# Performance work log

Hardware: AMD Instinct MI355X
Metric: run time of the kernel (lower is better)

Reference implementation:

```python
import jax, jax.numpy as jnp
import numpy as np

N_LAYERS = 6
D_MODEL = 512
D_FFN = 2048
N_STATE = 64
KSIZE = 31
BATCH = 8
SEQ = 2048
IN_SIZE = 80


def _ln(x, g, b, eps=1e-5):
    m = jnp.mean(x, axis=-1, keepdims=True)
    v = jnp.mean((x - m) ** 2, axis=-1, keepdims=True)
    return (x - m) * jax.lax.rsqrt(v + eps) * g + b


def _ffn(x, g, b, w1, b1, w2, b2):
    # LayerNorm -> Linear(D->F) -> GELU -> Linear(F->D)  (PositionalwiseFeedForward)
    h = jax.nn.gelu(_ln(x, g, b) @ w1 + b1)
    return h @ w2 + b2


def _dss(x, lam_re, lam_im, c_re, c_im, d_skip, log_dt, w_out, b_out):
    # Diagonal state-space (DSS-EXP): generate length-T kernel from diagonal poles,
    # apply causal conv via FFT, skip D*u, GELU, GLU output projection.
    Bx, T, H = x.shape
    dt = jnp.exp(log_dt)
    lam = -jnp.exp(lam_re) + 1j * lam_im                        # [N] stable poles (Re<0)
    P = jnp.exp(lam[:, None] * (dt * jnp.arange(T))[None, :])   # [N, T]
    C = c_re + 1j * c_im                                        # [H, N]
    kern = jnp.einsum('hn,nt->ht', C, P).real * dt              # [H, T]
    u = x.transpose(0, 2, 1)                                    # [B, H, T]
    n = 2 * T
    y = jnp.fft.irfft(jnp.fft.rfft(u, n=n) * jnp.fft.rfft(kern, n=n), n=n)[..., :T]
    y = y + d_skip[None, :, None] * u
    y = jax.nn.gelu(y.transpose(0, 2, 1))                       # [B, T, H]
    z = y @ w_out + b_out                                       # [B, T, 2H]
    a, g = jnp.split(z, 2, axis=-1)
    return a * jax.nn.sigmoid(g)                                # GLU


def _conv_module(x, g1, b1, bw, bb, dw, db, g2, b2, lw, lb):
    # LN -> 1x1 conv to 2D + GLU -> depthwise conv (SAME, k=31) -> LN -> GELU -> Linear
    y = _ln(x, g1, b1)
    y = y @ bw.T + bb                                           # [B, T, 2D]
    a, g = jnp.split(y, 2, axis=-1)
    y = a * jax.nn.sigmoid(g)                                   # GLU over channels
    yc = y.transpose(0, 2, 1)                                   # [B, D, T]
    yc = jax.lax.conv_general_dilated(
        yc, dw[:, None, :], (1,), 'SAME',
        feature_group_count=yc.shape[1],
        dimension_numbers=('NCH', 'OIH', 'NCH'))
    yc = yc + db[None, :, None]
    y = jax.nn.gelu(_ln(yc.transpose(0, 2, 1), g2, b2))
    return y @ lw.T + lb


def _forward(src, speaker_embs, src_w, src_b,
             ffn1_ln_g, ffn1_ln_b, ffn1_w1, ffn1_b1, ffn1_w2, ffn1_b2,
             norm1_g, norm1_b,
             lam_re, lam_im, c_re, c_im, ssm_d, log_dt, dss_out_w, dss_out_b,
             conv_ln_g, conv_ln_b, bneck_w, bneck_b, dw_w, dw_b,
             conv_ln2_g, conv_ln2_b, conv_lin_w, conv_lin_b,
             ffn2_ln_g, ffn2_ln_b, ffn2_w1, ffn2_b1, ffn2_w2, ffn2_b2,
             norm2_g, norm2_b, final_g, final_b):
    x = src @ src_w + src_b                                     # custom_src_module Linear
    for i in range(N_LAYERS):
        x = x + 0.5 * _ffn(x, ffn1_ln_g[i], ffn1_ln_b[i], ffn1_w1[i], ffn1_b1[i], ffn1_w2[i], ffn1_b2[i])
        skip = x
        x = _ln(x, norm1_g[i], norm1_b[i])
        x = _dss(x, lam_re[i], lam_im[i], c_re[i], c_im[i], ssm_d[i], log_dt[i], dss_out_w[i], dss_out_b[i])
        x = x + skip
        x = x + _conv_module(x, conv_ln_g[i], conv_ln_b[i], bneck_w[i], bneck_b[i], dw_w[i], dw_b[i],
                             conv_ln2_g[i], conv_ln2_b[i], conv_lin_w[i], conv_lin_b[i])
        x = _ln(x + 0.5 * _ffn(x, ffn2_ln_g[i], ffn2_ln_b[i], ffn2_w1[i], ffn2_b1[i], ffn2_w2[i], ffn2_b2[i]),
                norm2_g[i], norm2_b[i])
    x = _ln(x, final_g, final_b, eps=1e-6)
    return x + speaker_embs


def setup_inputs() -> dict:
    key = jax.random.key(0)
    ks = iter(jax.random.split(key, 64))
    def rn(shape, s=0.02):
        return (jax.random.normal(next(ks), shape) * s).astype(jnp.float32)
    L, D, F, N, K = N_LAYERS, D_MODEL, D_FFN, N_STATE, KSIZE
    return dict(
        src=jax.random.normal(next(ks), (BATCH, SEQ, IN_SIZE), dtype=jnp.float32),
        speaker_embs=jax.random.normal(next(ks), (BATCH, 1, D), dtype=jnp.float32),
        src_w=rn((IN_SIZE, D)), src_b=jnp.zeros((D,), jnp.float32),
        ffn1_ln_g=jnp.ones((L, D), jnp.float32), ffn1_ln_b=jnp.zeros((L, D), jnp.float32),
        ffn1_w1=rn((L, D, F)), ffn1_b1=jnp.zeros((L, F), jnp.float32),
        ffn1_w2=rn((L, F, D)), ffn1_b2=jnp.zeros((L, D), jnp.float32),
        norm1_g=jnp.ones((L, D), jnp.float32), norm1_b=jnp.zeros((L, D), jnp.float32),
        lam_re=rn((L, N), 0.5), lam_im=rn((L, N), 3.0),
        c_re=rn((L, D, N), 0.1), c_im=rn((L, D, N), 0.1),
        ssm_d=rn((L, D), 1.0), log_dt=jnp.full((L,), float(np.log(0.01)), jnp.float32),
        dss_out_w=rn((L, D, 2 * D)), dss_out_b=jnp.zeros((L, 2 * D), jnp.float32),
        conv_ln_g=jnp.ones((L, D), jnp.float32), conv_ln_b=jnp.zeros((L, D), jnp.float32),
        bneck_w=rn((L, 2 * D, D)), bneck_b=jnp.zeros((L, 2 * D), jnp.float32),
        dw_w=rn((L, D, K), 0.1), dw_b=jnp.zeros((L, D), jnp.float32),
        conv_ln2_g=jnp.ones((L, D), jnp.float32), conv_ln2_b=jnp.zeros((L, D), jnp.float32),
        conv_lin_w=rn((L, D, D)), conv_lin_b=jnp.zeros((L, D), jnp.float32),
        ffn2_ln_g=jnp.ones((L, D), jnp.float32), ffn2_ln_b=jnp.zeros((L, D), jnp.float32),
        ffn2_w1=rn((L, D, F)), ffn2_b1=jnp.zeros((L, F), jnp.float32),
        ffn2_w2=rn((L, F, D)), ffn2_b2=jnp.zeros((L, D), jnp.float32),
        norm2_g=jnp.ones((L, D), jnp.float32), norm2_b=jnp.zeros((L, D), jnp.float32),
        final_g=jnp.ones((D,), jnp.float32), final_b=jnp.zeros((D,), jnp.float32),
    )


def reference(src, speaker_embs, src_w, src_b,
              ffn1_ln_g, ffn1_ln_b, ffn1_w1, ffn1_b1, ffn1_w2, ffn1_b2,
              norm1_g, norm1_b,
              lam_re, lam_im, c_re, c_im, ssm_d, log_dt, dss_out_w, dss_out_b,
              conv_ln_g, conv_ln_b, bneck_w, bneck_b, dw_w, dw_b,
              conv_ln2_g, conv_ln2_b, conv_lin_w, conv_lin_b,
              ffn2_ln_g, ffn2_ln_b, ffn2_w1, ffn2_b1, ffn2_w2, ffn2_b2,
              norm2_g, norm2_b, final_g, final_b):
    return _forward(src, speaker_embs, src_w, src_b,
                    ffn1_ln_g, ffn1_ln_b, ffn1_w1, ffn1_b1, ffn1_w2, ffn1_b2,
                    norm1_g, norm1_b,
                    lam_re, lam_im, c_re, c_im, ssm_d, log_dt, dss_out_w, dss_out_b,
                    conv_ln_g, conv_ln_b, bneck_w, bneck_b, dw_w, dw_b,
                    conv_ln2_g, conv_ln2_b, conv_lin_w, conv_lin_b,
                    ffn2_ln_g, ffn2_ln_b, ffn2_w1, ffn2_b1, ffn2_w2, ffn2_b2,
                    norm2_g, norm2_b, final_g, final_b)
```

## Files before the change

kernel.cpp:

```cpp
#include <hip/hip_runtime.h>
#include <hip/hip_bf16.h>
#include <stdint.h>


#define NL 6
#define TT 2048
#define BB 8
#define DD 512
#define FF 2048
#define ROWS (BB*TT)

typedef __attribute__((ext_vector_type(4))) float f32x4;
typedef __attribute__((ext_vector_type(8))) short s16x8;

#define DEVI __device__ __forceinline__

DEVI float bf2f(uint32_t u) { union { uint32_t i; float f; } v; v.i = u << 16; return v.f; }
DEVI uint16_t f2bf(float f) {
    union { float f; uint32_t i; } v; v.f = f;
    uint32_t x = v.i;
    return (uint16_t)((x + 0x7fffu + ((x >> 16) & 1u)) >> 16);
}
DEVI float gelu_f(float x) {
    float x2 = x * x;
    float z  = x * fmaf(x2, 0.07135481627f, 1.5957691216f);
    return x * __builtin_amdgcn_rcpf(1.0f + __expf(-z));
}
DEVI float sigm(float x) { return __builtin_amdgcn_rcpf(1.0f + __expf(-x)); }

DEVI void gload16(const uint16_t* g, uint16_t* l) {
    __builtin_amdgcn_global_load_lds((const __attribute__((address_space(1))) void*)g,
                                     (__attribute__((address_space(3))) void*)l, 16, 0, 0);
}

__global__ void k_wtrans(const float* __restrict__ src, uint16_t* __restrict__ dst,
                         int K, int N) {
    __shared__ float tile[32][33];
    int l = blockIdx.z;
    const float* s = src + (size_t)l * K * N;
    uint16_t*    d = dst + (size_t)l * N * K;
    int n0 = blockIdx.x * 32, k0 = blockIdx.y * 32;
    int tx = threadIdx.x, ty = threadIdx.y;
#pragma unroll
    for (int i = 0; i < 4; i++) {
        int k = k0 + ty + i * 8;
        tile[ty + i * 8][tx] = s[(size_t)k * N + n0 + tx];
    }
    __syncthreads();
#pragma unroll
    for (int i = 0; i < 4; i++) {
        int n = n0 + ty + i * 8;
        d[(size_t)n * K + k0 + tx] = f2bf(tile[tx][ty + i * 8]);
    }
}
__global__ void k_wcvt(const float* __restrict__ src, uint16_t* __restrict__ dst, int n) {
    int i = blockIdx.x * 256 + threadIdx.x;
    if (i < n) dst[i] = f2bf(src[i]);
}
__global__ void k_dwt(const float* __restrict__ dw, float* __restrict__ dwt) {
    int i = blockIdx.x * 256 + threadIdx.x;
    int tot = NL * DD * 31;
    if (i >= tot) return;
    int l = i / (DD * 31), r = i % (DD * 31), d = r / 31, k = r % 31;
    dwt[(size_t)l * 31 * DD + k * DD + d] = dw[i];
}
__global__ void k_srcpad(const float* __restrict__ src, uint16_t* __restrict__ dst) {
    int i = blockIdx.x * 256 + threadIdx.x;
    if (i >= ROWS * 96) return;
    int r = i / 96, c = i - r * 96;
    dst[i] = (c < 80) ? f2bf(src[(size_t)r * 80 + c]) : (uint16_t)0;
}
__global__ void k_wsrcpad(const float* __restrict__ w, uint16_t* __restrict__ dst) {
    int i = blockIdx.x * 256 + threadIdx.x;
    if (i >= DD * 96) return;
    int n = i / 96, k = i - n * 96;
    dst[i] = (k < 80) ? f2bf(w[(size_t)k * DD + n]) : (uint16_t)0;
}

template <int MODE>
__global__ void k_ln(const float* __restrict__ in, void* __restrict__ outp,
                     const float* __restrict__ gam, const float* __restrict__ bet,
                     const float* __restrict__ spk, float eps) {
    int row  = blockIdx.x * 4 + (threadIdx.x >> 6);
    int lane = threadIdx.x & 63;
    const float* x = in + (size_t)row * DD;
    float4 a0 = *(const float4*)&x[lane * 4];
    float4 a1 = *(const float4*)&x[256 + lane * 4];
    float v[8] = {a0.x, a0.y, a0.z, a0.w, a1.x, a1.y, a1.z, a1.w};
    float s = 0.f, q = 0.f;
#pragma unroll
    for (int i = 0; i < 8; i++) { s += v[i]; q += v[i] * v[i]; }
#pragma unroll
    for (int m = 1; m < 64; m <<= 1) { s += __shfl_xor(s, m); q += __shfl_xor(q, m); }
    float mean = s * (1.0f / 512.0f);
    float var  = fmaxf(q * (1.0f / 512.0f) - mean * mean, 0.0f);
    float inv  = rsqrtf(var + eps);
    float4 g0 = *(const float4*)&gam[lane * 4];
    float4 g1 = *(const float4*)&gam[256 + lane * 4];
    float4 b0 = *(const float4*)&bet[lane * 4];
    float4 b1 = *(const float4*)&bet[256 + lane * 4];
    float gv[8] = {g0.x, g0.y, g0.z, g0.w, g1.x, g1.y, g1.z, g1.w};
    float bv[8] = {b0.x, b0.y, b0.z, b0.w, b1.x, b1.y, b1.z, b1.w};
    float y[8];
#pragma unroll
    for (int i = 0; i < 8; i++) y[i] = (v[i] - mean) * inv * gv[i] + bv[i];
    if (MODE == 1) {
#pragma unroll
        for (int i = 0; i < 8; i++) y[i] = gelu_f(y[i]);
    }
    if (MODE == 0 || MODE == 1) {
        uint16_t* o = (uint16_t*)outp + (size_t)row * DD;
        uint2 p0, p1;
        p0.x = (uint32_t)f2bf(y[0]) | ((uint32_t)f2bf(y[1]) << 16);
        p0.y = (uint32_t)f2bf(y[2]) | ((uint32_t)f2bf(y[3]) << 16);
        p1.x = (uint32_t)f2bf(y[4]) | ((uint32_t)f2bf(y[5]) << 16);
        p1.y = (uint32_t)f2bf(y[6]) | ((uint32_t)f2bf(y[7]) << 16);
        *(uint2*)&o[lane * 4]       = p0;
        *(uint2*)&o[256 + lane * 4] = p1;
    } else {
        float* o = (float*)outp + (size_t)row * DD;
        if (MODE == 3) {
            const float* sp = spk + (size_t)(row >> 11) * DD;
            float4 s0 = *(const float4*)&sp[lane * 4];
            float4 s1 = *(const float4*)&sp[256 + lane * 4];
            y[0] += s0.x; y[1] += s0.y; y[2] += s0.z; y[3] += s0.w;
            y[4] += s1.x; y[5] += s1.y; y[6] += s1.z; y[7] += s1.w;
        }
        *(float4*)&o[lane * 4]       = make_float4(y[0], y[1], y[2], y[3]);
        *(float4*)&o[256 + lane * 4] = make_float4(y[4], y[5], y[6], y[7]);
    }
}

template <int MODE>
__global__ __launch_bounds__(256) void k_gemm(
    const uint16_t* __restrict__ A, const uint16_t* __restrict__ Bt,
    const float* __restrict__ bias, int M, int N, int K,
    void* __restrict__ outp, float* __restrict__ X) {
    __shared__ __align__(16) uint16_t As[2][128 * 32];
    __shared__ __align__(16) uint16_t Bs[2][128 * 32];
    int tid = threadIdx.x;
    int m0 = blockIdx.x * 128, n0 = blockIdx.y * 128;
    int wave = tid >> 6, lane = tid & 63;
    int wm = (wave >> 1) * 64, wn = (wave & 1) * 64;
    int l15 = lane & 15, l16 = lane >> 4;

    const uint16_t* gA = A  + (size_t)(m0 + 32 * wave + l15) * K + l16 * 8;
    const uint16_t* gB = Bt + (size_t)(n0 + 32 * wave + l15) * K + l16 * 8;
    size_t rowskip = (size_t)16 * K;

    f32x4 acc[4][4];
#pragma unroll
    for (int i = 0; i < 4; i++)
#pragma unroll
        for (int j = 0; j < 4; j++) acc[i][j] = (f32x4){0.f, 0.f, 0.f, 0.f};

    gload16(gA, &As[0][(2 * wave) * 512]);
    gload16(gA + rowskip, &As[0][(2 * wave + 1) * 512]);
    gload16(gB, &Bs[0][(2 * wave) * 512]);
    gload16(gB + rowskip, &Bs[0][(2 * wave + 1) * 512]);
    __syncthreads();

    int nk = K >> 5;
    for (int it = 0; it < nk; ++it) {
        int cur = it & 1;
        if (it + 1 < nk) {
            int kt = (it + 1) << 5;
            gload16(gA + kt, &As[cur ^ 1][(2 * wave) * 512]);
            gload16(gA + rowskip + kt, &As[cur ^ 1][(2 * wave + 1) * 512]);
            gload16(gB + kt, &Bs[cur ^ 1][(2 * wave) * 512]);
            gload16(gB + rowskip + kt, &Bs[cur ^ 1][(2 * wave + 1) * 512]);
        }
        s16x8 af[4], bfr[4];
#pragma unroll
        for (int i = 0; i < 4; i++)
            af[i] = *(const s16x8*)&As[cur][((wave >> 1) * 4 + i) * 512 + lane * 8];
#pragma unroll
        for (int j = 0; j < 4; j++)
            bfr[j] = *(const s16x8*)&Bs[cur][((wave & 1) * 4 + j) * 512 + lane * 8];
#pragma unroll
        for (int i = 0; i < 4; i++)
#pragma unroll
            for (int j = 0; j < 4; j++)
                acc[i][j] = __builtin_amdgcn_mfma_f32_16x16x32_bf16(af[i], bfr[j], acc[i][j], 0, 0, 0);
        __syncthreads();
    }
#pragma unroll
    for (int i = 0; i < 4; i++) {
#pragma unroll
        for (int j = 0; j < 4; j++) {
            int gcol = n0 + wn + j * 16 + l15;
            float bv = bias[gcol];
#pragma unroll
            for (int q = 0; q < 4; q++) {
                int grow = m0 + wm + i * 16 + l16 * 4 + q;
                float v = acc[i][j][q] + bv;
                if (MODE == 0) {
                    ((uint16_t*)outp)[(size_t)grow * N + gcol] = f2bf(gelu_f(v));
                } else if (MODE == 1) {
                    ((uint16_t*)outp)[(size_t)grow * N + gcol] = f2bf(v);
                } else if (MODE == 2) {
                    X[(size_t)grow * DD + gcol] += 0.5f * v;
                } else if (MODE == 3) {
                    X[(size_t)grow * DD + gcol] += v;
                } else if (MODE == 4) {
                    ((float*)outp)[(size_t)grow * DD + gcol] =
                        X[(size_t)grow * DD + gcol] + 0.5f * v;
                } else {
                    X[(size_t)grow * DD + gcol] = v;
                }
            }
        }
    }
}

__global__ void k_tpose(const uint16_t* __restrict__ in, uint16_t* __restrict__ out,
                        int R, int C) {
    __shared__ uint16_t tile[32][33];
    size_t boff = (size_t)blockIdx.z * R * C;
    int c0 = blockIdx.x * 32, r0 = blockIdx.y * 32;
    int tx = threadIdx.x, ty = threadIdx.y;
#pragma unroll
    for (int i = 0; i < 4; i++)
        tile[ty + i * 8][tx] = in[boff + (size_t)(r0 + ty + i * 8) * C + c0 + tx];
    __syncthreads();
#pragma unroll
    for (int i = 0; i < 4; i++)
        out[boff + (size_t)(c0 + ty + i * 8) * R + r0 + tx] = tile[tx][ty + i * 8];
}


__global__ __launch_bounds__(64) void k_phiprep(
        const float* __restrict__ lam_re, const float* __restrict__ lam_im,
        const float* __restrict__ log_dt, uint16_t* __restrict__ PHI,
        float* __restrict__ A64f) {
    int l = blockIdx.x, n = threadIdx.x;
    float dt = expf(log_dt[l]);
    float lr = lam_re[l * 64 + n], li = lam_im[l * 64 + n];
    float mag = expf(-expf(lr) * dt), th = li * dt;
    float Are = mag * __cosf(th), Aim = mag * __sinf(th);
    float Pre = 1.f, Pim = 0.f;
    uint16_t* ph = PHI + (size_t)l * 8192;
    for (int tau = 0; tau < 64; tau++) {
        int s = 63 - tau;
        ph[n * 64 + s]        = f2bf(Pre);
        ph[(64 + n) * 64 + s] = f2bf(Pim);
        float nr = Pre * Are - Pim * Aim;
        float ni = Pre * Aim + Pim * Are;
        Pre = nr; Pim = ni;
    }
    A64f[l * 128 + 2 * n]     = Pre;
    A64f[l * 128 + 2 * n + 1] = Pim;
}

__global__ __launch_bounds__(64) void k_gprep(
        const float* __restrict__ lam_re, const float* __restrict__ lam_im,
        const float* __restrict__ c_re, const float* __restrict__ c_im,
        const float* __restrict__ ssm_d, const float* __restrict__ log_dt,
        int l, uint16_t* __restrict__ G) {
    int h = blockIdx.x, n = threadIdx.x;
    __shared__ float klds[64];
    float dt = expf(log_dt[l]);
    float lr = lam_re[l * 64 + n], li = lam_im[l * 64 + n];
    float mag = expf(-expf(lr) * dt), th = li * dt;
    float Are = mag * __cosf(th), Aim = mag * __sinf(th);
    float Cre = c_re[(size_t)l * DD * 64 + h * 64 + n];
    float Cim = c_im[(size_t)l * DD * 64 + h * 64 + n];
    uint16_t* Gh = G + (size_t)h * 64 * 192;
    float Pre = 1.f, Pim = 0.f;
    for (int r = 0; r < 64; r++) {
        float t = Cre * Pre - Cim * Pim;
        float s = t;
        s += __shfl_xor(s, 1);  s += __shfl_xor(s, 2);  s += __shfl_xor(s, 4);
        s += __shfl_xor(s, 8);  s += __shfl_xor(s, 16); s += __shfl_xor(s, 32);
        if (n == 0) klds[r] = dt * s;
        float nr = Pre * Are - Pim * Aim;
        float ni = Pre * Aim + Pim * Are;
        float wre = dt * (Cre * nr - Cim * ni);
        float wim = dt * (Cre * ni + Cim * nr);
        Gh[r * 192 + 64 + n]  = f2bf(wre);
        Gh[r * 192 + 128 + n] = f2bf(-wim);
        Pre = nr; Pim = ni;
    }
    __syncthreads();
    float dh = ssm_d[l * DD + h];
    for (int r = 0; r < 64; r++) {
        int c = n;
        float val = (c < r) ? klds[r - c] : (c == r ? klds[0] + dh : 0.f);
        Gh[r * 192 + c] = f2bf(val);
    }
}

__global__ __launch_bounds__(256) void k_pass1(
        const uint16_t* __restrict__ u, const uint16_t* __restrict__ PHI,
        uint16_t* __restrict__ E) {
    __shared__ __align__(16) uint16_t Phs[128 * 72];
    int tid = threadIdx.x;
    for (int v = tid; v < 1024; v += 256) {
        int row = v >> 3, kb = v & 7;
        *(s16x8*)&Phs[row * 72 + kb * 8] = *(const s16x8*)&PHI[row * 64 + kb * 8];
    }
    __syncthreads();
    int wave = tid >> 6, lane = tid & 63;
    int l15 = lane & 15, l16 = lane >> 4;
    int m0 = (wave & 1) * 64;
    int colbase = blockIdx.x * 128 + (wave >> 1) * 64;
    f32x4 acc[4][4];
#pragma unroll
    for (int i = 0; i < 4; i++)
#pragma unroll
        for (int j = 0; j < 4; j++) acc[i][j] = (f32x4){0.f, 0.f, 0.f, 0.f};
#pragma unroll
    for (int kt = 0; kt < 64; kt += 32) {
        s16x8 a[4], b[4];
#pragma unroll
        for (int i = 0; i < 4; i++)
            a[i] = *(const s16x8*)&Phs[(m0 + i * 16 + l15) * 72 + kt + l16 * 8];
#pragma unroll
        for (int j = 0; j < 4; j++)
            b[j] = *(const s16x8*)(u + (size_t)(colbase + j * 16 + l15) * 64 + kt + l16 * 8);
#pragma unroll
        for (int i = 0; i < 4; i++)
#pragma unroll
            for (int j = 0; j < 4; j++)
                acc[i][j] = __builtin_amdgcn_mfma_f32_16x16x32_bf16(a[i], b[j], acc[i][j], 0, 0, 0);
    }
#pragma unroll
    for (int i = 0; i < 4; i++)
#pragma unroll
        for (int j = 0; j < 4; j++) {
            int col = colbase + j * 16 + l15;
            int r0  = m0 + i * 16 + l16 * 4;
            uint32_t p0 = (uint32_t)f2bf(acc[i][j][0]) | ((uint32_t)f2bf(acc[i][j][1]) << 16);
            uint32_t p1 = (uint32_t)f2bf(acc[i][j][2]) | ((uint32_t)f2bf(acc[i][j][3]) << 16);
            *(uint2*)&E[(size_t)col * 128 + r0] = make_uint2(p0, p1);
        }
}

__global__ void k_pass2(const uint16_t* __restrict__ E, const float* __restrict__ A64f,
                        int l, uint16_t* __restrict__ Sp) {
    int gid = blockIdx.x * 256 + threadIdx.x;
    int n = gid & 63, bh = gid >> 6;
    int b = bh >> 9, h = bh & 511;
    float2 A = *(const float2*)&A64f[l * 128 + 2 * n];
    float Sre = 0.f, Sim = 0.f;
    const uint16_t* Eb = E + (size_t)bh * 32 * 128;
    uint16_t* So = Sp + (size_t)h * 32768 + (size_t)b * 32 * 128;
    for (int i = 0; i < 32; i++) {
        So[i * 128 + n]      = f2bf(Sre);
        So[i * 128 + 64 + n] = f2bf(Sim);
        float er = bf2f((uint32_t)Eb[i * 128 + n]);
        float ei = bf2f((uint32_t)Eb[i * 128 + 64 + n]);
        float nr = A.x * Sre - A.y * Sim + er;
        float ni = A.x * Sim + A.y * Sre + ei;
        Sre = nr; Sim = ni;
    }
}

__global__ __launch_bounds__(256) void k_pass3(
        const uint16_t* __restrict__ G, const uint16_t* __restrict__ u,
        const uint16_t* __restrict__ Sp, uint16_t* __restrict__ Y) {
    __shared__ __align__(16) uint16_t Gs[64 * 200];
    int h = blockIdx.x, tid = threadIdx.x;
    for (int v = tid; v < 1536; v += 256) {
        int row = v / 24, kb = v % 24;
        *(s16x8*)&Gs[row * 200 + kb * 8] = *(const s16x8*)&G[(size_t)h * 12288 + row * 192 + kb * 8];
    }
    __syncthreads();
    int wave = tid >> 6, lane = tid & 63;
    int l15 = lane & 15, l16 = lane >> 4;
    int wn = wave * 64;
    const uint16_t* uh = u + (size_t)h * TT;
    const uint16_t* sh = Sp + (size_t)h * 32768;
    f32x4 acc[4][4];
#pragma unroll
    for (int i = 0; i < 4; i++)
#pragma unroll
        for (int j = 0; j < 4; j++) acc[i][j] = (f32x4){0.f, 0.f, 0.f, 0.f};
#pragma unroll
    for (int kt = 0; kt < 192; kt += 32) {
        s16x8 a[4], b[4];
#pragma unroll
        for (int i = 0; i < 4; i++)
            a[i] = *(const s16x8*)&Gs[(i * 16 + l15) * 200 + kt + l16 * 8];
#pragma unroll
        for (int j = 0; j < 4; j++) {
            int col = wn + j * 16 + l15;
            const uint16_t* src;
            if (kt < 64)
                src = uh + (size_t)(col >> 5) * (DD * TT) + (col & 31) * 64 + kt + l16 * 8;
            else
                src = sh + (size_t)col * 128 + (kt - 64) + l16 * 8;
            b[j] = *(const s16x8*)src;
        }
#pragma unroll
        for (int i = 0; i < 4; i++)
#pragma unroll
            for (int j = 0; j < 4; j++)
                acc[i][j] = __builtin_amdgcn_mfma_f32_16x16x32_bf16(a[i], b[j], acc[i][j], 0, 0, 0);
    }
#pragma unroll
    for (int i = 0; i < 4; i++)
#pragma unroll
        for (int j = 0; j < 4; j++) {
            int col = wn + j * 16 + l15;
            int r0  = i * 16 + l16 * 4;
            uint16_t* dst = Y + (size_t)(col >> 5) * (DD * TT) + (size_t)h * TT + (col & 31) * 64 + r0;
            uint32_t p0 = (uint32_t)f2bf(acc[i][j][0]) | ((uint32_t)f2bf(acc[i][j][1]) << 16);
            uint32_t p1 = (uint32_t)f2bf(acc[i][j][2]) | ((uint32_t)f2bf(acc[i][j][3]) << 16);
            *(uint2*)&dst[0] = make_uint2(p0, p1);
        }
}

__global__ void k_tgelu(const uint16_t* __restrict__ y, uint16_t* __restrict__ out) {
    __shared__ uint16_t tile[32][33];
    int b = blockIdx.z;
    int t0 = blockIdx.x * 32, h0 = blockIdx.y * 32;
    int tx = threadIdx.x, ty = threadIdx.y;
    const uint16_t* yb = y + (size_t)b * DD * TT;
#pragma unroll
    for (int i = 0; i < 4; i++) {
        int h = h0 + ty + i * 8;
        tile[ty + i * 8][tx] = f2bf(gelu_f(bf2f((uint32_t)yb[(size_t)h * TT + t0 + tx])));
    }
    __syncthreads();
    uint16_t* ob = out + (size_t)b * TT * DD;
#pragma unroll
    for (int i = 0; i < 4; i++) {
        int t = t0 + ty + i * 8;
        ob[(size_t)t * DD + h0 + tx] = tile[tx][ty + i * 8];
    }
}

template <int SKIP>
__global__ void k_glu(const uint16_t* __restrict__ z, float* __restrict__ X,
                      uint16_t* __restrict__ out) {
    int i = blockIdx.x * 256 + threadIdx.x;
    int r = i >> 8;
    int c = (i & 255) * 2;
    uint32_t av = *(const uint32_t*)&z[(size_t)r * 1024 + c];
    uint32_t gv = *(const uint32_t*)&z[(size_t)r * 1024 + 512 + c];
    float a0 = bf2f(av & 0xffffu), a1 = bf2f(av >> 16);
    float g0 = bf2f(gv & 0xffffu), g1 = bf2f(gv >> 16);
    float v0 = a0 * sigm(g0), v1 = a1 * sigm(g1);
    if (SKIP) {
        float2* px = (float2*)&X[(size_t)r * DD + c];
        float2 x = *px;
        x.x += v0; x.y += v1;
        *px = x;
    } else {
        uint32_t p = (uint32_t)f2bf(v0) | ((uint32_t)f2bf(v1) << 16);
        *(uint32_t*)&out[(size_t)r * DD + c] = p;
    }
}

__global__ __launch_bounds__(256) void k_dwconv(
        const uint16_t* __restrict__ in, const float* __restrict__ dwt,
        const float* __restrict__ db, float* __restrict__ out) {
    __shared__ __align__(16) uint16_t xs[34 * 512];
    int tid = threadIdx.x;
    int t0 = (blockIdx.x & 511) * 4;
    int b  = blockIdx.x >> 9;
    const uint16_t* ib = in + (size_t)b * TT * DD;
    for (int v = tid; v < 34 * 64; v += 256) {
        int row = v >> 6, seg = v & 63;
        int tj = t0 - 15 + row;
        uint4 val = make_uint4(0, 0, 0, 0);
        if (tj >= 0 && tj < TT) val = *(const uint4*)&ib[(size_t)tj * DD + seg * 8];
        *(uint4*)&xs[row * 512 + seg * 8] = val;
    }
    __syncthreads();
    int d = tid * 2;
    float a0[4], a1[4];
    float bv0 = db[d], bv1 = db[d + 1];
#pragma unroll
    for (int o = 0; o < 4; o++) { a0[o] = bv0; a1[o] = bv1; }
#pragma unroll
    for (int k = 0; k < 31; k++) {
        float2 w = *(const float2*)&dwt[k * DD + d];
#pragma unroll
        for (int o = 0; o < 4; o++) {
            uint32_t v = *(const uint32_t*)&xs[(o + k) * 512 + d];
            a0[o] = fmaf(bf2f(v & 0xffffu), w.x, a0[o]);
            a1[o] = fmaf(bf2f(v >> 16), w.y, a1[o]);
        }
    }
#pragma unroll
    for (int o = 0; o < 4; o++) {
        *(float2*)&out[((size_t)b * TT + t0 + o) * DD + d] = make_float2(a0[o], a1[o]);
    }
}

extern "C" void kernel_launch(void* const* d_in, const int* in_sizes, int n_in,
                              void* d_out, int out_size, void* d_ws, size_t ws_size,
                              hipStream_t stream) {
    const float* src        = (const float*)d_in[0];
    const float* speaker    = (const float*)d_in[1];
    const float* src_w      = (const float*)d_in[2];
    const float* src_b      = (const float*)d_in[3];
    const float* ffn1_ln_g  = (const float*)d_in[4];
    const float* ffn1_ln_b  = (const float*)d_in[5];
    const float* ffn1_w1    = (const float*)d_in[6];
    const float* ffn1_b1    = (const float*)d_in[7];
    const float* ffn1_w2    = (const float*)d_in[8];
    const float* ffn1_b2    = (const float*)d_in[9];
    const float* norm1_g    = (const float*)d_in[10];
    const float* norm1_b    = (const float*)d_in[11];
    const float* lam_re     = (const float*)d_in[12];
    const float* lam_im     = (const float*)d_in[13];
    const float* c_re       = (const float*)d_in[14];
    const float* c_im       = (const float*)d_in[15];
    const float* ssm_d      = (const float*)d_in[16];
    const float* log_dt     = (const float*)d_in[17];
    const float* dss_out_w  = (const float*)d_in[18];
    const float* dss_out_b  = (const float*)d_in[19];
    const float* conv_ln_g  = (const float*)d_in[20];
    const float* conv_ln_b  = (const float*)d_in[21];
    const float* bneck_w    = (const float*)d_in[22];
    const float* bneck_b    = (const float*)d_in[23];
    const float* dw_w       = (const float*)d_in[24];
    const float* dw_b       = (const float*)d_in[25];
    const float* conv_ln2_g = (const float*)d_in[26];
    const float* conv_ln2_b = (const float*)d_in[27];
    const float* conv_lin_w = (const float*)d_in[28];
    const float* conv_lin_b = (const float*)d_in[29];
    const float* ffn2_ln_g  = (const float*)d_in[30];
    const float* ffn2_ln_b  = (const float*)d_in[31];
    const float* ffn2_w1    = (const float*)d_in[32];
    const float* ffn2_b1    = (const float*)d_in[33];
    const float* ffn2_w2    = (const float*)d_in[34];
    const float* ffn2_b2    = (const float*)d_in[35];
    const float* norm2_g    = (const float*)d_in[36];
    const float* norm2_b    = (const float*)d_in[37];
    const float* final_g    = (const float*)d_in[38];
    const float* final_b    = (const float*)d_in[39];
    (void)in_sizes; (void)n_in; (void)out_size; (void)ws_size;

    uint8_t* ws = (uint8_t*)d_ws;
    float*    X   = (float*)   (ws + 0);
    float*    F0  = (float*)   (ws + 33554432);
    uint16_t* B1  = (uint16_t*)(ws + 67108864);
    uint16_t* B2  = (uint16_t*)(ws + 83886080);
    uint16_t* B3  = (uint16_t*)(ws + 100663296);
    uint16_t* H   = (uint16_t*)(ws + 117440512);
    uint16_t* Wf1a= (uint16_t*)(ws + 184549376);
    uint16_t* Wf1b= (uint16_t*)(ws + 197132288);
    uint16_t* Wds = (uint16_t*)(ws + 209715200);
    uint16_t* Wbn = (uint16_t*)(ws + 216006656);
    uint16_t* Wcl = (uint16_t*)(ws + 222298112);
    uint16_t* Wf2a= (uint16_t*)(ws + 225443840);
    uint16_t* Wf2b= (uint16_t*)(ws + 238026752);
    float*    DWT = (float*)   (ws + 250609664);
    uint16_t* PHI = (uint16_t*)(ws + 250990592);
    float*    A64f= (float*)   (ws + 251088896);

    uint16_t* GBUF = B1;
    uint16_t* SPK  = (uint16_t*)F0;
    uint16_t* EBUF = H;
    uint16_t* SRCB = B3;
    uint16_t* WSRC = B2;

    dim3 tb(32, 8);
    k_wtrans<<<dim3(FF/32, DD/32, NL), tb, 0, stream>>>(ffn1_w1, Wf1a, DD, FF);
    k_wtrans<<<dim3(DD/32, FF/32, NL), tb, 0, stream>>>(ffn1_w2, Wf1b, FF, DD);
    k_wtrans<<<dim3(1024/32, DD/32, NL), tb, 0, stream>>>(dss_out_w, Wds, DD, 1024);
    k_wcvt<<<(NL*1024*DD + 255)/256, 256, 0, stream>>>(bneck_w, Wbn, NL*1024*DD);
    k_wcvt<<<(NL*DD*DD + 255)/256, 256, 0, stream>>>(conv_lin_w, Wcl, NL*DD*DD);
    k_wtrans<<<dim3(FF/32, DD/32, NL), tb, 0, stream>>>(ffn2_w1, Wf2a, DD, FF);
    k_wtrans<<<dim3(DD/32, FF/32, NL), tb, 0, stream>>>(ffn2_w2, Wf2b, FF, DD);
    k_dwt<<<(NL*DD*31 + 255)/256, 256, 0, stream>>>(dw_w, DWT);
    k_phiprep<<<NL, 64, 0, stream>>>(lam_re, lam_im, log_dt, PHI, A64f);
    k_srcpad<<<(ROWS*96 + 255)/256, 256, 0, stream>>>(src, SRCB);
    k_wsrcpad<<<(DD*96 + 255)/256, 256, 0, stream>>>(src_w, WSRC);

    k_gemm<5><<<dim3(128, 4), 256, 0, stream>>>(SRCB, WSRC, src_b, ROWS, DD, 96, nullptr, X);

    for (int l = 0; l < NL; l++) {
        k_ln<0><<<4096, 256, 0, stream>>>(X, B1, ffn1_ln_g + l*DD, ffn1_ln_b + l*DD, nullptr, 1e-5f);
        k_gemm<0><<<dim3(128, 16), 256, 0, stream>>>(B1, Wf1a + (size_t)l*FF*DD, ffn1_b1 + l*FF,
                                                     ROWS, FF, DD, H, nullptr);
        k_gemm<2><<<dim3(128, 4), 256, 0, stream>>>(H, Wf1b + (size_t)l*DD*FF, ffn1_b2 + l*DD,
                                                    ROWS, DD, FF, nullptr, X);
        k_ln<0><<<4096, 256, 0, stream>>>(X, B1, norm1_g + l*DD, norm1_b + l*DD, nullptr, 1e-5f);
        k_tpose<<<dim3(DD/32, TT/32, BB), tb, 0, stream>>>(B1, B2, TT, DD);
        k_gprep<<<DD, 64, 0, stream>>>(lam_re, lam_im, c_re, c_im, ssm_d, log_dt, l, GBUF);
        k_pass1<<<1024, 256, 0, stream>>>(B2, PHI + (size_t)l*8192, EBUF);
        k_pass2<<<1024, 256, 0, stream>>>(EBUF, A64f, l, SPK);
        k_pass3<<<DD, 256, 0, stream>>>(GBUF, B2, SPK, B3);
        k_tgelu<<<dim3(TT/32, DD/32, BB), tb, 0, stream>>>(B3, B1);
        k_gemm<1><<<dim3(128, 8), 256, 0, stream>>>(B1, Wds + (size_t)l*1024*DD, dss_out_b + l*1024,
                                                    ROWS, 1024, DD, H, nullptr);
        k_glu<1><<<ROWS, 256, 0, stream>>>(H, X, nullptr);
        k_ln<0><<<4096, 256, 0, stream>>>(X, B1, conv_ln_g + l*DD, conv_ln_b + l*DD, nullptr, 1e-5f);
        k_gemm<1><<<dim3(128, 8), 256, 0, stream>>>(B1, Wbn + (size_t)l*1024*DD, bneck_b + l*1024,
                                                    ROWS, 1024, DD, H, nullptr);
        k_glu<0><<<ROWS, 256, 0, stream>>>(H, nullptr, B2);
        k_dwconv<<<BB*512, 256, 0, stream>>>(B2, DWT + (size_t)l*31*DD, dw_b + l*DD, F0);
        k_ln<1><<<4096, 256, 0, stream>>>(F0, B1, conv_ln2_g + l*DD, conv_ln2_b + l*DD, nullptr, 1e-5f);
        k_gemm<3><<<dim3(128, 4), 256, 0, stream>>>(B1, Wcl + (size_t)l*DD*DD, conv_lin_b + l*DD,
                                                    ROWS, DD, DD, nullptr, X);
        k_ln<0><<<4096, 256, 0, stream>>>(X, B1, ffn2_ln_g + l*DD, ffn2_ln_b + l*DD, nullptr, 1e-5f);
        k_gemm<0><<<dim3(128, 16), 256, 0, stream>>>(B1, Wf2a + (size_t)l*FF*DD, ffn2_b1 + l*FF,
                                                     ROWS, FF, DD, H, nullptr);
        k_gemm<4><<<dim3(128, 4), 256, 0, stream>>>(H, Wf2b + (size_t)l*DD*FF, ffn2_b2 + l*DD,
                                                    ROWS, DD, FF, F0, X);
        k_ln<2><<<4096, 256, 0, stream>>>(F0, X, norm2_g + l*DD, norm2_b + l*DD, nullptr, 1e-5f);
    }
    k_ln<3><<<4096, 256, 0, stream>>>(X, d_out, final_g, final_b, speaker, 1e-6f);
}
```

Baseline: 3.675 ms.

## Use larger 256-row GEMM tiles and fuse GLU, depthwise conv and LayerNorm kernels

Replaces the 128x128, 256-thread GEMM with a templated 512-thread kernel using 256-row tiles, 128- or 256-column tiles and a 64-wide K step. This raises operand reuse and halves the number of K iterations. It also fuses several elementwise passes: GLU residual with the following LayerNorm, depthwise conv with LN+GELU, and the norm2 LN with the next layer's FFN1 LN or the final LN. The input projection is padded to K=128 so it fits the new GEMM. The larger tiles use more LDS and registers, which may lower occupancy, and the fused kernels add block-level reductions.

```diff
diff --git a/kernel.cpp b/kernel.cpp
--- a/kernel.cpp
+++ b/kernel.cpp
@@ -66,14 +66,14 @@
 }
 __global__ void k_srcpad(const float* __restrict__ src, uint16_t* __restrict__ dst) {
     int i = blockIdx.x * 256 + threadIdx.x;
-    if (i >= ROWS * 96) return;
-    int r = i / 96, c = i - r * 96;
+    if (i >= ROWS * 128) return;
+    int r = i >> 7, c = i & 127;
     dst[i] = (c < 80) ? f2bf(src[(size_t)r * 80 + c]) : (uint16_t)0;
 }
 __global__ void k_wsrcpad(const float* __restrict__ w, uint16_t* __restrict__ dst) {
     int i = blockIdx.x * 256 + threadIdx.x;
-    if (i >= DD * 96) return;
-    int n = i / 96, k = i - n * 96;
+    if (i >= DD * 128) return;
+    int n = i >> 7, k = i & 127;
     dst[i] = (k < 80) ? f2bf(w[(size_t)k * DD + n]) : (uint16_t)0;
 }
 
@@ -104,95 +104,224 @@
     float y[8];
 #pragma unroll
     for (int i = 0; i < 8; i++) y[i] = (v[i] - mean) * inv * gv[i] + bv[i];
-    if (MODE == 1) {
-#pragma unroll
-        for (int i = 0; i < 8; i++) y[i] = gelu_f(y[i]);
-    }
-    if (MODE == 0 || MODE == 1) {
-        uint16_t* o = (uint16_t*)outp + (size_t)row * DD;
+    uint16_t* o = (uint16_t*)outp + (size_t)row * DD;
+    uint2 p0, p1;
+    p0.x = (uint32_t)f2bf(y[0]) | ((uint32_t)f2bf(y[1]) << 16);
+    p0.y = (uint32_t)f2bf(y[2]) | ((uint32_t)f2bf(y[3]) << 16);
+    p1.x = (uint32_t)f2bf(y[4]) | ((uint32_t)f2bf(y[5]) << 16);
+    p1.y = (uint32_t)f2bf(y[6]) | ((uint32_t)f2bf(y[7]) << 16);
+    *(uint2*)&o[lane * 4]       = p0;
+    *(uint2*)&o[256 + lane * 4] = p1;
+}
+
+template <int M2>
+__global__ void k_ln2(const float* __restrict__ in, float* __restrict__ X,
+                      void* __restrict__ out2,
+                      const float* __restrict__ g1, const float* __restrict__ b1,
+                      const float* __restrict__ g2, const float* __restrict__ b2,
+                      const float* __restrict__ spk, float eps2) {
+    int row  = blockIdx.x * 4 + (threadIdx.x >> 6);
+    int lane = threadIdx.x & 63;
+    const float* x = in + (size_t)row * DD;
+    float4 a0 = *(const float4*)&x[lane * 4];
+    float4 a1 = *(const float4*)&x[256 + lane * 4];
+    float v[8] = {a0.x, a0.y, a0.z, a0.w, a1.x, a1.y, a1.z, a1.w};
+    float s = 0.f, q = 0.f;
+#pragma unroll
+    for (int i = 0; i < 8; i++) { s += v[i]; q += v[i] * v[i]; }
+#pragma unroll
+    for (int m = 1; m < 64; m <<= 1) { s += __shfl_xor(s, m); q += __shfl_xor(q, m); }
+    float mean = s * (1.0f / 512.0f);
+    float var  = fmaxf(q * (1.0f / 512.0f) - mean * mean, 0.0f);
+    float inv  = rsqrtf(var + 1e-5f);
+    float4 g0 = *(const float4*)&g1[lane * 4];
+    float4 g1v = *(const float4*)&g1[256 + lane * 4];
+    float4 b0 = *(const float4*)&b1[lane * 4];
+    float4 b1v = *(const float4*)&b1[256 + lane * 4];
+    float gv[8] = {g0.x, g0.y, g0.z, g0.w, g1v.x, g1v.y, g1v.z, g1v.w};
+    float bv[8] = {b0.x, b0.y, b0.z, b0.w, b1v.x, b1v.y, b1v.z, b1v.w};
+    float y[8];
+    float s2 = 0.f, q2 = 0.f;
+#pragma unroll
+    for (int i = 0; i < 8; i++) {
+        y[i] = (v[i] - mean) * inv * gv[i] + bv[i];
+        s2 += y[i]; q2 += y[i] * y[i];
+    }
+    if (M2 == 6) {
+        float* xo = X + (size_t)row * DD;
+        *(float4*)&xo[lane * 4]       = make_float4(y[0], y[1], y[2], y[3]);
+        *(float4*)&xo[256 + lane * 4] = make_float4(y[4], y[5], y[6], y[7]);
+    }
+#pragma unroll
+    for (int m = 1; m < 64; m <<= 1) { s2 += __shfl_xor(s2, m); q2 += __shfl_xor(q2, m); }
+    float mean2 = s2 * (1.0f / 512.0f);
+    float var2  = fmaxf(q2 * (1.0f / 512.0f) - mean2 * mean2, 0.0f);
+    float inv2  = rsqrtf(var2 + eps2);
+    float4 G0 = *(const float4*)&g2[lane * 4];
+    float4 G1 = *(const float4*)&g2[256 + lane * 4];
+    float4 B0 = *(const float4*)&b2[lane * 4];
+    float4 B1v = *(const float4*)&b2[256 + lane * 4];
+    float Gv[8] = {G0.x, G0.y, G0.z, G0.w, G1.x, G1.y, G1.z, G1.w};
+    float Bv[8] = {B0.x, B0.y, B0.z, B0.w, B1v.x, B1v.y, B1v.z, B1v.w};
+    float z[8];
+#pragma unroll
+    for (int i = 0; i < 8; i++) z[i] = (y[i] - mean2) * inv2 * Gv[i] + Bv[i];
+    if (M2 == 6) {
+        uint16_t* o = (uint16_t*)out2 + (size_t)row * DD;
         uint2 p0, p1;
-        p0.x = (uint32_t)f2bf(y[0]) | ((uint32_t)f2bf(y[1]) << 16);
-        p0.y = (uint32_t)f2bf(y[2]) | ((uint32_t)f2bf(y[3]) << 16);
-        p1.x = (uint32_t)f2bf(y[4]) | ((uint32_t)f2bf(y[5]) << 16);
-        p1.y = (uint32_t)f2bf(y[6]) | ((uint32_t)f2bf(y[7]) << 16);
+        p0.x = (uint32_t)f2bf(z[0]) | ((uint32_t)f2bf(z[1]) << 16);
+        p0.y = (uint32_t)f2bf(z[2]) | ((uint32_t)f2bf(z[3]) << 16);
+        p1.x = (uint32_t)f2bf(z[4]) | ((uint32_t)f2bf(z[5]) << 16);
+        p1.y = (uint32_t)f2bf(z[6]) | ((uint32_t)f2bf(z[7]) << 16);
         *(uint2*)&o[lane * 4]       = p0;
         *(uint2*)&o[256 + lane * 4] = p1;
     } else {
-        float* o = (float*)outp + (size_t)row * DD;
-        if (MODE == 3) {
-            const float* sp = spk + (size_t)(row >> 11) * DD;
-            float4 s0 = *(const float4*)&sp[lane * 4];
-            float4 s1 = *(const float4*)&sp[256 + lane * 4];
-            y[0] += s0.x; y[1] += s0.y; y[2] += s0.z; y[3] += s0.w;
-            y[4] += s1.x; y[5] += s1.y; y[6] += s1.z; y[7] += s1.w;
-        }
-        *(float4*)&o[lane * 4]       = make_float4(y[0], y[1], y[2], y[3]);
-        *(float4*)&o[256 + lane * 4] = make_float4(y[4], y[5], y[6], y[7]);
-    }
-}
-
-template <int MODE>
-__global__ __launch_bounds__(256) void k_gemm(
+        const float* sp = spk + (size_t)(row >> 11) * DD;
+        float4 s0 = *(const float4*)&sp[lane * 4];
+        float4 s1 = *(const float4*)&sp[256 + lane * 4];
+        float* o = (float*)out2 + (size_t)row * DD;
+        *(float4*)&o[lane * 4]       = make_float4(z[0]+s0.x, z[1]+s0.y, z[2]+s0.z, z[3]+s0.w);
+        *(float4*)&o[256 + lane * 4] = make_float4(z[4]+s1.x, z[5]+s1.y, z[6]+s1.z, z[7]+s1.w);
+    }
+}
+
+__global__ void k_gluln(const uint16_t* __restrict__ H, float* __restrict__ X,
+                        uint16_t* __restrict__ out,
+                        const float* __restrict__ gam, const float* __restrict__ bet) {
+    int row  = blockIdx.x * 4 + (threadIdx.x >> 6);
+    int lane = threadIdx.x & 63;
+    const uint16_t* hr = H + (size_t)row * 1024;
+    uint2 ha0 = *(const uint2*)&hr[lane * 4];
+    uint2 ha1 = *(const uint2*)&hr[256 + lane * 4];
+    uint2 hg0 = *(const uint2*)&hr[512 + lane * 4];
+    uint2 hg1 = *(const uint2*)&hr[768 + lane * 4];
+    uint32_t aw[4] = {ha0.x, ha0.y, ha1.x, ha1.y};
+    uint32_t gw[4] = {hg0.x, hg0.y, hg1.x, hg1.y};
+    float* xr = X + (size_t)row * DD;
+    float4 x0 = *(const float4*)&xr[lane * 4];
+    float4 x1 = *(const float4*)&xr[256 + lane * 4];
+    float xv[8] = {x0.x, x0.y, x0.z, x0.w, x1.x, x1.y, x1.z, x1.w};
+    float v[8];
+#pragma unroll
+    for (int p = 0; p < 4; p++) {
+        float a0 = bf2f(aw[p] & 0xffffu), a1 = bf2f(aw[p] >> 16);
+        float g0 = bf2f(gw[p] & 0xffffu), g1 = bf2f(gw[p] >> 16);
+        v[2*p]   = xv[2*p]   + a0 * sigm(g0);
+        v[2*p+1] = xv[2*p+1] + a1 * sigm(g1);
+    }
+    *(float4*)&xr[lane * 4]       = make_float4(v[0], v[1], v[2], v[3]);
+    *(float4*)&xr[256 + lane * 4] = make_float4(v[4], v[5], v[6], v[7]);
+    float s = 0.f, q = 0.f;
+#pragma unroll
+    for (int i = 0; i < 8; i++) { s += v[i]; q += v[i] * v[i]; }
+#pragma unroll
+    for (int m = 1; m < 64; m <<= 1) { s += __shfl_xor(s, m); q += __shfl_xor(q, m); }
+    float mean = s * (1.0f / 512.0f);
+    float var  = fmaxf(q * (1.0f / 512.0f) - mean * mean, 0.0f);
+    float inv  = rsqrtf(var + 1e-5f);
+    float4 g0 = *(const float4*)&gam[lane * 4];
+    float4 g1 = *(const float4*)&gam[256 + lane * 4];
+    float4 b0 = *(const float4*)&bet[lane * 4];
+    float4 b1 = *(const float4*)&bet[256 + lane * 4];
+    float gv[8] = {g0.x, g0.y, g0.z, g0.w, g1.x, g1.y, g1.z, g1.w};
+    float bv[8] = {b0.x, b0.y, b0.z, b0.w, b1.x, b1.y, b1.z, b1.w};
+    uint16_t* o = out + (size_t)row * DD;
+    uint2 p0, p1;
+    float y0 = (v[0]-mean)*inv*gv[0]+bv[0], y1 = (v[1]-mean)*inv*gv[1]+bv[1];
+    float y2 = (v[2]-mean)*inv*gv[2]+bv[2], y3 = (v[3]-mean)*inv*gv[3]+bv[3];
+    float y4 = (v[4]-mean)*inv*gv[4]+bv[4], y5 = (v[5]-mean)*inv*gv[5]+bv[5];
+    float y6 = (v[6]-mean)*inv*gv[6]+bv[6], y7 = (v[7]-mean)*inv*gv[7]+bv[7];
+    p0.x = (uint32_t)f2bf(y0) | ((uint32_t)f2bf(y1) << 16);
+    p0.y = (uint32_t)f2bf(y2) | ((uint32_t)f2bf(y3) << 16);
+    p1.x = (uint32_t)f2bf(y4) | ((uint32_t)f2bf(y5) << 16);
+    p1.y = (uint32_t)f2bf(y6) | ((uint32_t)f2bf(y7) << 16);
+    *(uint2*)&o[lane * 4]       = p0;
+    *(uint2*)&o[256 + lane * 4] = p1;
+}
+
+template <int MODE, int WM, int WN, int BN>
+__global__ __launch_bounds__(512) void k_gemm2(
     const uint16_t* __restrict__ A, const uint16_t* __restrict__ Bt,
     const float* __restrict__ bias, int M, int N, int K,
     void* __restrict__ outp, float* __restrict__ X) {
-    __shared__ __align__(16) uint16_t As[2][128 * 32];
-    __shared__ __align__(16) uint16_t Bs[2][128 * 32];
+    constexpr int BM = 256;
+    constexpr int MR = BM / WM / 16;
+    constexpr int NR = BN / WN / 16;
+    constexpr int ABLK = (BM / 16) * 2;
+    constexpr int BBLK = (BN / 16) * 2;
+    constexpr int APW = ABLK / 8;
+    constexpr int BPW = BBLK / 8;
+    __shared__ __align__(16) uint16_t As[2][ABLK * 512];
+    __shared__ __align__(16) uint16_t Bs[2][BBLK * 512];
     int tid = threadIdx.x;
-    int m0 = blockIdx.x * 128, n0 = blockIdx.y * 128;
     int wave = tid >> 6, lane = tid & 63;
-    int wm = (wave >> 1) * 64, wn = (wave & 1) * 64;
     int l15 = lane & 15, l16 = lane >> 4;
-
-    const uint16_t* gA = A  + (size_t)(m0 + 32 * wave + l15) * K + l16 * 8;
-    const uint16_t* gB = Bt + (size_t)(n0 + 32 * wave + l15) * K + l16 * 8;
-    size_t rowskip = (size_t)16 * K;
-
-    f32x4 acc[4][4];
-#pragma unroll
-    for (int i = 0; i < 4; i++)
-#pragma unroll
-        for (int j = 0; j < 4; j++) acc[i][j] = (f32x4){0.f, 0.f, 0.f, 0.f};
-
-    gload16(gA, &As[0][(2 * wave) * 512]);
-    gload16(gA + rowskip, &As[0][(2 * wave + 1) * 512]);
-    gload16(gB, &Bs[0][(2 * wave) * 512]);
-    gload16(gB + rowskip, &Bs[0][(2 * wave + 1) * 512]);
-    __syncthreads();
-
-    int nk = K >> 5;
+    int wr = wave / WN, wc = wave % WN;
+    int m0 = blockIdx.x * BM, n0 = blockIdx.y * BN;
+
+    const uint16_t* srcA[APW];
+    const uint16_t* srcB[BPW];
+#pragma unroll
+    for (int p = 0; p < APW; p++) {
+        int bi = wave * APW + p, rb = bi >> 1, ks = bi & 1;
+        srcA[p] = A + (size_t)(m0 + rb * 16 + l15) * K + ks * 32 + l16 * 8;
+    }
+#pragma unroll
+    for (int p = 0; p < BPW; p++) {
+        int bi = wave * BPW + p, rb = bi >> 1, ks = bi & 1;
+        srcB[p] = Bt + (size_t)(n0 + rb * 16 + l15) * K + ks * 32 + l16 * 8;
+    }
+
+    f32x4 acc[MR][NR];
+#pragma unroll
+    for (int i = 0; i < MR; i++)
+#pragma unroll
+        for (int j = 0; j < NR; j++) acc[i][j] = (f32x4){0.f, 0.f, 0.f, 0.f};
+
+#pragma unroll
+    for (int p = 0; p < APW; p++) gload16(srcA[p], &As[0][(wave * APW + p) * 512]);
+#pragma unroll
+    for (int p = 0; p < BPW; p++) gload16(srcB[p], &Bs[0][(wave * BPW + p) * 512]);
+    __syncthreads();
+
+    int nk = K >> 6;
     for (int it = 0; it < nk; ++it) {
         int cur = it & 1;
         if (it + 1 < nk) {
-            int kt = (it + 1) << 5;
-            gload16(gA + kt, &As[cur ^ 1][(2 * wave) * 512]);
-            gload16(gA + rowskip + kt, &As[cur ^ 1][(2 * wave + 1) * 512]);
-            gload16(gB + kt, &Bs[cur ^ 1][(2 * wave) * 512]);
-            gload16(gB + rowskip + kt, &Bs[cur ^ 1][(2 * wave + 1) * 512]);
+            int kt = (it + 1) << 6;
+#pragma unroll
+            for (int p = 0; p < APW; p++)
+                gload16(srcA[p] + kt, &As[cur ^ 1][(wave * APW + p) * 512]);
+#pragma unroll
+            for (int p = 0; p < BPW; p++)
+                gload16(srcB[p] + kt, &Bs[cur ^ 1][(wave * BPW + p) * 512]);
         }
-        s16x8 af[4], bfr[4];
-#pragma unroll
-        for (int i = 0; i < 4; i++)
-            af[i] = *(const s16x8*)&As[cur][((wave >> 1) * 4 + i) * 512 + lane * 8];
-#pragma unroll
-        for (int j = 0; j < 4; j++)
-            bfr[j] = *(const s16x8*)&Bs[cur][((wave & 1) * 4 + j) * 512 + lane * 8];
-#pragma unroll
-        for (int i = 0; i < 4; i++)
-#pragma unroll
-            for (int j = 0; j < 4; j++)
-                acc[i][j] = __builtin_amdgcn_mfma_f32_16x16x32_bf16(af[i], bfr[j], acc[i][j], 0, 0, 0);
+#pragma unroll
+        for (int s = 0; s < 2; s++) {
+            s16x8 af[MR], bfr[NR];
+#pragma unroll
+            for (int i = 0; i < MR; i++)
+                af[i] = *(const s16x8*)&As[cur][((wr * MR + i) * 2 + s) * 512 + lane * 8];
+#pragma unroll
+            for (int j = 0; j < NR; j++)
+                bfr[j] = *(const s16x8*)&Bs[cur][((wc * NR + j) * 2 + s) * 512 + lane * 8];
+#pragma unroll
+            for (int i = 0; i < MR; i++)
+#pragma unroll
+                for (int j = 0; j < NR; j++)
+                    acc[i][j] = __builtin_amdgcn_mfma_f32_16x16x32_bf16(af[i], bfr[j], acc[i][j], 0, 0, 0);
+        }
         __syncthreads();
     }
 #pragma unroll
-    for (int i = 0; i < 4; i++) {
-#pragma unroll
-        for (int j = 0; j < 4; j++) {
-            int gcol = n0 + wn + j * 16 + l15;
+    for (int i = 0; i < MR; i++) {
+#pragma unroll
+        for (int j = 0; j < NR; j++) {
+            int gcol = n0 + wc * NR * 16 + j * 16 + l15;
             float bv = bias[gcol];
 #pragma unroll
             for (int q = 0; q < 4; q++) {
-                int grow = m0 + wm + i * 16 + l16 * 4 + q;
+                int grow = m0 + wr * MR * 16 + i * 16 + l16 * 4 + q;
                 float v = acc[i][j][q] + bv;
                 if (MODE == 0) {
                     ((uint16_t*)outp)[(size_t)grow * N + gcol] = f2bf(gelu_f(v));
@@ -227,7 +356,6 @@
     for (int i = 0; i < 4; i++)
         out[boff + (size_t)(c0 + ty + i * 8) * R + r0 + tx] = tile[tx][ty + i * 8];
 }
-
 
 __global__ __launch_bounds__(64) void k_phiprep(
         const float* __restrict__ lam_re, const float* __restrict__ lam_im,
@@ -431,9 +559,7 @@
     }
 }
 
-template <int SKIP>
-__global__ void k_glu(const uint16_t* __restrict__ z, float* __restrict__ X,
-                      uint16_t* __restrict__ out) {
+__global__ void k_glu(const uint16_t* __restrict__ z, uint16_t* __restrict__ out) {
     int i = blockIdx.x * 256 + threadIdx.x;
     int r = i >> 8;
     int c = (i & 255) * 2;
@@ -442,21 +568,16 @@
     float a0 = bf2f(av & 0xffffu), a1 = bf2f(av >> 16);
     float g0 = bf2f(gv & 0xffffu), g1 = bf2f(gv >> 16);
     float v0 = a0 * sigm(g0), v1 = a1 * sigm(g1);
-    if (SKIP) {
-        float2* px = (float2*)&X[(size_t)r * DD + c];
-        float2 x = *px;
-        x.x += v0; x.y += v1;
-        *px = x;
-    } else {
-        uint32_t p = (uint32_t)f2bf(v0) | ((uint32_t)f2bf(v1) << 16);
-        *(uint32_t*)&out[(size_t)r * DD + c] = p;
-    }
-}
-
-__global__ __launch_bounds__(256) void k_dwconv(
+    uint32_t p = (uint32_t)f2bf(v0) | ((uint32_t)f2bf(v1) << 16);
+    *(uint32_t*)&out[(size_t)r * DD + c] = p;
+}
+
+__global__ __launch_bounds__(256) void k_dwln(
         const uint16_t* __restrict__ in, const float* __restrict__ dwt,
-        const float* __restrict__ db, float* __restrict__ out) {
+        const float* __restrict__ db, const float* __restrict__ gam,
+        const float* __restrict__ bet, uint16_t* __restrict__ out) {
     __shared__ __align__(16) uint16_t xs[34 * 512];
+    __shared__ float red[4][4][2];
     int tid = threadIdx.x;
     int t0 = (blockIdx.x & 511) * 4;
     int b  = blockIdx.x >> 9;
@@ -470,6 +591,7 @@
     }
     __syncthreads();
     int d = tid * 2;
+    int wave = tid >> 6, lane = tid & 63;
     float a0[4], a1[4];
     float bv0 = db[d], bv1 = db[d + 1];
 #pragma unroll
@@ -486,7 +608,25 @@
     }
 #pragma unroll
     for (int o = 0; o < 4; o++) {
-        *(float2*)&out[((size_t)b * TT + t0 + o) * DD + d] = make_float2(a0[o], a1[o]);
+        float ss = a0[o] + a1[o];
+        float qq = a0[o] * a0[o] + a1[o] * a1[o];
+#pragma unroll
+        for (int m = 1; m < 64; m <<= 1) { ss += __shfl_xor(ss, m); qq += __shfl_xor(qq, m); }
+        if (lane == 0) { red[o][wave][0] = ss; red[o][wave][1] = qq; }
+    }
+    __syncthreads();
+    float g0 = gam[d], g1 = gam[d + 1], be0 = bet[d], be1 = bet[d + 1];
+#pragma unroll
+    for (int o = 0; o < 4; o++) {
+        float s = red[o][0][0] + red[o][1][0] + red[o][2][0] + red[o][3][0];
+        float q = red[o][0][1] + red[o][1][1] + red[o][2][1] + red[o][3][1];
+        float mean = s * (1.0f / 512.0f);
+        float var  = fmaxf(q * (1.0f / 512.0f) - mean * mean, 0.0f);
+        float inv  = rsqrtf(var + 1e-5f);
+        float y0 = gelu_f((a0[o] - mean) * inv * g0 + be0);
+        float y1 = gelu_f((a1[o] - mean) * inv * g1 + be1);
+        uint32_t p = (uint32_t)f2bf(y0) | ((uint32_t)f2bf(y1) << 16);
+        *(uint32_t*)&out[((size_t)b * TT + t0 + o) * DD + d] = p;
     }
 }
 
@@ -569,17 +709,17 @@
     k_wtrans<<<dim3(DD/32, FF/32, NL), tb, 0, stream>>>(ffn2_w2, Wf2b, FF, DD);
     k_dwt<<<(NL*DD*31 + 255)/256, 256, 0, stream>>>(dw_w, DWT);
     k_phiprep<<<NL, 64, 0, stream>>>(lam_re, lam_im, log_dt, PHI, A64f);
-    k_srcpad<<<(ROWS*96 + 255)/256, 256, 0, stream>>>(src, SRCB);
-    k_wsrcpad<<<(DD*96 + 255)/256, 256, 0, stream>>>(src_w, WSRC);
-
-    k_gemm<5><<<dim3(128, 4), 256, 0, stream>>>(SRCB, WSRC, src_b, ROWS, DD, 96, nullptr, X);
+    k_srcpad<<<(ROWS*128 + 255)/256, 256, 0, stream>>>(src, SRCB);
+    k_wsrcpad<<<(DD*128 + 255)/256, 256, 0, stream>>>(src_w, WSRC);
+
+    k_gemm2<5,4,2,128><<<dim3(64, 4), 512, 0, stream>>>(SRCB, WSRC, src_b, ROWS, DD, 128, nullptr, X);
+    k_ln<0><<<4096, 256, 0, stream>>>(X, B1, ffn1_ln_g, ffn1_ln_b, nullptr, 1e-5f);
 
     for (int l = 0; l < NL; l++) {
-        k_ln<0><<<4096, 256, 0, stream>>>(X, B1, ffn1_ln_g + l*DD, ffn1_ln_b + l*DD, nullptr, 1e-5f);
-        k_gemm<0><<<dim3(128, 16), 256, 0, stream>>>(B1, Wf1a + (size_t)l*FF*DD, ffn1_b1 + l*FF,
-                                                     ROWS, FF, DD, H, nullptr);
-        k_gemm<2><<<dim3(128, 4), 256, 0, stream>>>(H, Wf1b + (size_t)l*DD*FF, ffn1_b2 + l*DD,
-                                                    ROWS, DD, FF, nullptr, X);
+        k_gemm2<0,2,4,256><<<dim3(64, 8), 512, 0, stream>>>(B1, Wf1a + (size_t)l*FF*DD, ffn1_b1 + l*FF,
+                                                            ROWS, FF, DD, H, nullptr);
+        k_gemm2<2,4,2,128><<<dim3(64, 4), 512, 0, stream>>>(H, Wf1b + (size_t)l*DD*FF, ffn1_b2 + l*DD,
+                                                            ROWS, DD, FF, nullptr, X);
         k_ln<0><<<4096, 256, 0, stream>>>(X, B1, norm1_g + l*DD, norm1_b + l*DD, nullptr, 1e-5f);
         k_tpose<<<dim3(DD/32, TT/32, BB), tb, 0, stream>>>(B1, B2, TT, DD);
         k_gprep<<<DD, 64, 0, stream>>>(lam_re, lam_im, c_re, c_im, ssm_d, log_dt, l, GBUF);
@@ -587,23 +727,28 @@
         k_pass2<<<1024, 256, 0, stream>>>(EBUF, A64f, l, SPK);
         k_pass3<<<DD, 256, 0, stream>>>(GBUF, B2, SPK, B3);
         k_tgelu<<<dim3(TT/32, DD/32, BB), tb, 0, stream>>>(B3, B1);
-        k_gemm<1><<<dim3(128, 8), 256, 0, stream>>>(B1, Wds + (size_t)l*1024*DD, dss_out_b + l*1024,
-                                                    ROWS, 1024, DD, H, nullptr);
-        k_glu<1><<<ROWS, 256, 0, stream>>>(H, X, nullptr);
-        k_ln<0><<<4096, 256, 0, stream>>>(X, B1, conv_ln_g + l*DD, conv_ln_b + l*DD, nullptr, 1e-5f);
-        k_gemm<1><<<dim3(128, 8), 256, 0, stream>>>(B1, Wbn + (size_t)l*1024*DD, bneck_b + l*1024,
-                                                    ROWS, 1024, DD, H, nullptr);
-        k_glu<0><<<ROWS, 256, 0, stream>>>(H, nullptr, B2);
-        k_dwconv<<<BB*512, 256, 0, stream>>>(B2, DWT + (size_t)l*31*DD, dw_b + l*DD, F0);
-        k_ln<1><<<4096, 256, 0, stream>>>(F0, B1, conv_ln2_g + l*DD, conv_ln2_b + l*DD, nullptr, 1e-5f);
-        k_gemm<3><<<dim3(128, 4), 256, 0, stream>>>(B1, Wcl + (size_t)l*DD*DD, conv_lin_b + l*DD,
-                                                    ROWS, DD, DD, nullptr, X);
+        k_gemm2<1,2,4,256><<<dim3(64, 4), 512, 0, stream>>>(B1, Wds + (size_t)l*1024*DD, dss_out_b + l*1024,
+                                                            ROWS, 1024, DD, H, nullptr);
+        k_gluln<<<4096, 256, 0, stream>>>(H, X, B1, conv_ln_g + l*DD, conv_ln_b + l*DD);
+        k_gemm2<1,2,4,256><<<dim3(64, 4), 512, 0, stream>>>(B1, Wbn + (size_t)l*1024*DD, bneck_b + l*1024,
+                                                            ROWS, 1024, DD, H, nullptr);
+        k_glu<<<ROWS, 256, 0, stream>>>(H, B2);
+        k_dwln<<<BB*512, 256, 0, stream>>>(B2, DWT + (size_t)l*31*DD, dw_b + l*DD,
+                                           conv_ln2_g + l*DD, conv_ln2_b + l*DD, B1);
+        k_gemm2<3,4,2,128><<<dim3(64, 4), 512, 0, stream>>>(B1, Wcl + (size_t)l*DD*DD, conv_lin_b + l*DD,
+                                                            ROWS, DD, DD, nullptr, X);
         k_ln<0><<<4096, 256, 0, stream>>>(X, B1, ffn2_ln_g + l*DD, ffn2_ln_b + l*DD, nullptr, 1e-5f);
-        k_gemm<0><<<dim3(128, 16), 256, 0, stream>>>(B1, Wf2a + (size_t)l*FF*DD, ffn2_b1 + l*FF,
-                                                     ROWS, FF, DD, H, nullptr);
-        k_gemm<4><<<dim3(128, 4), 256, 0, stream>>>(H, Wf2b + (size_t)l*DD*FF, ffn2_b2 + l*DD,
-                                                    ROWS, DD, FF, F0, X);
-        k_ln<2><<<4096, 256, 0, stream>>>(F0, X, norm2_g + l*DD, norm2_b + l*DD, nullptr, 1e-5f);
-    }
-    k_ln<3><<<4096, 256, 0, stream>>>(X, d_out, final_g, final_b, speaker, 1e-6f);
-}
+        k_gemm2<0,2,4,256><<<dim3(64, 8), 512, 0, stream>>>(B1, Wf2a + (size_t)l*FF*DD, ffn2_b1 + l*FF,
+                                                            ROWS, FF, DD, H, nullptr);
+        k_gemm2<4,4,2,128><<<dim3(64, 4), 512, 0, stream>>>(H, Wf2b + (size_t)l*DD*FF, ffn2_b2 + l*DD,
+                                                            ROWS, DD, FF, F0, X);
+        if (l < NL - 1) {
+            k_ln2<6><<<4096, 256, 0, stream>>>(F0, X, B1, norm2_g + l*DD, norm2_b + l*DD,
+                                               ffn1_ln_g + (l+1)*DD, ffn1_ln_b + (l+1)*DD,
+                                               nullptr, 1e-5f);
+        } else {
+            k_ln2<7><<<4096, 256, 0, stream>>>(F0, nullptr, d_out, norm2_g + l*DD, norm2_b + l*DD,
+                                               final_g, final_b, speaker, 1e-6f);
+        }
+    }
+}
```

Result: faster. 3.403 ms (-7.4%).
